# Optimization experiments

Measured on AMD Instinct MI355X. Metric: run time of the kernel, lower is better.

The kernel has to match this reference:

```python
import jax, jax.numpy as jnp
import numpy as np

# Dims: C cells, L gene tokens, E embed, H mlp hidden, M factors, K topk
C, L, E, H, M, K = 16, 8192, 512, 256, 128, 30
TAU = 1.0        # gumbel-softmax temperature
SOFTNESS = 0.01  # soft-mask sharpness
TEMP = 1.0       # logits temperature
EPS = 1e-20


def setup_inputs() -> dict:
    key = jax.random.key(0)
    ks = jax.random.split(key, 7)
    x = jax.random.normal(ks[0], (C, L, E), dtype=jnp.float32)
    key_padding_mask = jax.random.randint(ks[1], (C, L), 0, 2) > 0  # True = valid
    uniform_noise = jax.random.uniform(ks[2], (C, L - 1, M), dtype=jnp.float32)
    W1 = jax.random.normal(ks[3], (E, H), dtype=jnp.float32) * (1.0 / np.sqrt(E))
    b1 = jnp.zeros((H,), dtype=jnp.float32)
    W2 = jax.random.normal(ks[4], (H, M), dtype=jnp.float32) * (1.0 / np.sqrt(H))
    b2 = jnp.zeros((M,), dtype=jnp.float32)
    return {"x": x, "key_padding_mask": key_padding_mask,
            "uniform_noise": uniform_noise,
            "W1": W1, "b1": b1, "W2": W2, "b2": b2}


def reference(x, key_padding_mask, uniform_noise, W1, b1, W2, b2):
    # default gene_subset: drop token 0, keep the rest  -> S = L-1
    xs = x[:, 1:, :]                          # (C, S, E)
    kpm = key_padding_mask[:, 1:]             # (C, S)

    # 2-layer MLP router (dropout p=0 -> identity)
    h = jax.nn.relu(jnp.einsum('cse,eh->csh', xs, W1) + b1)   # (C, S, H)
    logits = (jnp.einsum('csh,hm->csm', h, W2) + b2) / TEMP    # (C, S, M)

    # GumbelTopK, training path: gumbel-softmax then smooth top-k mask
    gumbel = -jnp.log(-jnp.log(uniform_noise + EPS) + EPS)
    perturbed = (logits + gumbel) / TAU
    probs = jax.nn.softmax(perturbed, axis=-1)                 # (C, S, M)
    topk_vals, _ = jax.lax.top_k(probs, K)                     # (C, S, K)
    threshold = topk_vals[..., -1:]                            # (C, S, 1)
    smooth_mask = jax.nn.sigmoid((probs - threshold) / SOFTNESS)
    out = probs * smooth_mask

    # faithful to the source: mask = ~key_padding_mask; probs *= mask
    out = out * (~kpm)[..., None].astype(out.dtype)
    return out, kpm
```

## Files before the change

kernel.cpp:

```cpp
#include <hip/hip_runtime.h>
#include <hip/hip_bf16.h>

#define CC 16
#define LL 8192
#define SS 8191
#define EE 512
#define HH 256
#define MM 128
#define TOPK 30

typedef __attribute__((ext_vector_type(8))) short short8;
typedef __attribute__((ext_vector_type(4))) float f32x4;
typedef __attribute__((ext_vector_type(4))) unsigned int u32x4;

static __device__ __forceinline__ unsigned short f2bf(float f) {
    unsigned u = __builtin_bit_cast(unsigned, f);
    u += 0x7FFFu + ((u >> 16) & 1u);
    return (unsigned short)(u >> 16);
}

static __device__ __forceinline__ unsigned pk2(float lo, float hi) {
    __hip_bfloat162 t = __float22bfloat162_rn(float2{lo, hi});
    unsigned u;
    __builtin_memcpy(&u, &t, 4);
    return u;
}

static __device__ __forceinline__ short8 cvt8(const float4 a, const float4 b) {
    u32x4 uv;
    uv[0] = pk2(a.x, a.y);
    uv[1] = pk2(a.z, a.w);
    uv[2] = pk2(b.x, b.y);
    uv[3] = pk2(b.z, b.w);
    return __builtin_bit_cast(short8, uv);
}

template<int CTRL>
static __device__ __forceinline__ float dppf(float v) {
    return __builtin_bit_cast(float,
        __builtin_amdgcn_update_dpp(0, __builtin_bit_cast(int, v), CTRL, 0xF, 0xF, false));
}
template<int CTRL>
static __device__ __forceinline__ int dppi(int v) {
    return __builtin_amdgcn_update_dpp(0, v, CTRL, 0xF, 0xF, false);
}
static __device__ __forceinline__ float sum16f(float v) {
    v += dppf<0x121>(v); v += dppf<0x122>(v); v += dppf<0x124>(v); v += dppf<0x128>(v);
    return v;
}
static __device__ __forceinline__ float max16f(float v) {
    v = fmaxf(v, dppf<0x121>(v)); v = fmaxf(v, dppf<0x122>(v));
    v = fmaxf(v, dppf<0x124>(v)); v = fmaxf(v, dppf<0x128>(v));
    return v;
}
static __device__ __forceinline__ int sum16i(int v) {
    v += dppi<0x121>(v); v += dppi<0x122>(v); v += dppi<0x124>(v); v += dppi<0x128>(v);
    return v;
}

__global__ void prep_weights(const float* __restrict__ W1, const float* __restrict__ W2,
                             unsigned short* __restrict__ W1T, unsigned short* __restrict__ W2T)
{
    const int b = blockIdx.x, tid = threadIdx.x;
    if (b < 64) {
        const int e0 = b * 8, h = tid;
        short8 sv;
#pragma unroll
        for (int j = 0; j < 8; ++j)
            sv[j] = (short)f2bf(W1[(size_t)(e0 + j) * HH + h]);
        *(short8*)(void*)(W1T + (size_t)h * EE + e0) = sv;
    } else {
        const int h0 = (b - 64) * 16;
        if (tid < MM) {
            const int m = tid;
            short8 s0v, s1v;
#pragma unroll
            for (int j = 0; j < 8; ++j) {
                s0v[j] = (short)f2bf(W2[(size_t)(h0 + j) * MM + m]);
                s1v[j] = (short)f2bf(W2[(size_t)(h0 + 8 + j) * MM + m]);
            }
            *(short8*)(void*)(W2T + (size_t)m * HH + h0) = s0v;
            *(short8*)(void*)(W2T + (size_t)m * HH + h0 + 8) = s1v;
        }
    }
}

__global__ __launch_bounds__(256, 4)
void gene_router_kernel(const float* __restrict__ x,
                        const int*   __restrict__ mask,
                        const float* __restrict__ noise,
                        const unsigned short* __restrict__ W1T,
                        const float* __restrict__ b1,
                        const unsigned short* __restrict__ W2T,
                        const float* __restrict__ b2,
                        float* __restrict__ out,
                        float* __restrict__ outk)
{
    __shared__ __align__(16) unsigned char lds[32768];
    float* sLf = (float*)lds;

    const int tid = threadIdx.x;
    const int c   = blockIdx.y;
    const int s0  = blockIdx.x * 32;

    const int w    = tid >> 6;
    const int lane = tid & 63;
    const int lr   = lane & 15;
    const int kq   = lane >> 4;
    const int tx   = tid & 15;
    const int ty   = tid >> 4;

    if (tid < 32) {
        const int s = s0 + tid;
        if (s < SS)
            outk[(size_t)c * SS + s] = (mask[(size_t)c * LL + s + 1] != 0) ? 1.0f : 0.0f;
    }

    const float* xb = x + ((size_t)c * LL + s0 + 1) * EE;
    const int rowA = tid >> 5;
    const int cu   = tid & 31;
#pragma unroll
    for (int it = 0; it < 4; ++it) {
        const int row = it * 8 + rowA;
        const int rs  = min(s0 + row, SS - 1) - s0;
        const float* p = xb + (size_t)rs * EE + cu * 8;
        const float4 a = *(const float4*)p;
        const float4 b = *(const float4*)(p + 4);
        *(short8*)(void*)(lds + row * 512 + ((cu * 16) ^ ((row & 7) << 4))) = cvt8(a, b);
    }
    __syncthreads();

    float4 rB[4][2];
#pragma unroll
    for (int it = 0; it < 4; ++it) {
        const int row = it * 8 + rowA;
        const int rs  = min(s0 + row, SS - 1) - s0;
        const float* p = xb + (size_t)rs * EE + 256 + cu * 8;
        rB[it][0] = *(const float4*)p;
        rB[it][1] = *(const float4*)(p + 4);
    }

    const int cw = w * 64;
    float b1v[4];
#pragma unroll
    for (int n = 0; n < 4; ++n) b1v[n] = b1[cw + n * 16 + lr];

    f32x4 acc[2][4];
#pragma unroll
    for (int r = 0; r < 2; ++r)
#pragma unroll
        for (int n = 0; n < 4; ++n) acc[r][n] = (f32x4)0.0f;

#pragma unroll 4
    for (int ks2 = 0; ks2 < 8; ++ks2) {
        short8 af[2];
#pragma unroll
        for (int r = 0; r < 2; ++r) {
            const int row = r * 16 + lr;
            af[r] = *(const short8*)(const void*)(lds + row * 512
                        + ((ks2 * 64 + kq * 16) ^ ((row & 7) << 4)));
        }
        short8 bf_[4];
#pragma unroll
        for (int n = 0; n < 4; ++n)
            bf_[n] = *(const short8*)(const void*)(W1T + (size_t)(cw + n * 16 + lr) * EE + ks2 * 32 + kq * 8);
#pragma unroll
        for (int r = 0; r < 2; ++r)
#pragma unroll
            for (int n = 0; n < 4; ++n)
                acc[r][n] = __builtin_amdgcn_mfma_f32_16x16x32_bf16(af[r], bf_[n], acc[r][n], 0, 0, 0);
    }

#pragma unroll
    for (int it = 0; it < 4; ++it) {
        const int row = it * 8 + rowA;
        *(short8*)(void*)(lds + 16384 + row * 512 + ((cu * 16) ^ ((row & 7) << 4)))
            = cvt8(rB[it][0], rB[it][1]);
    }
    __syncthreads();

    float4 nz[2][2];
    int mk[2];
#pragma unroll
    for (int i = 0; i < 2; ++i) {
        const int s  = s0 + ty * 2 + i;
        const int sc = min(s, SS - 1);
        const float* np_ = noise + ((size_t)c * SS + sc) * MM + tx * 8;
        nz[i][0] = *(const float4*)np_;
        nz[i][1] = *(const float4*)(np_ + 4);
        mk[i] = mask[(size_t)c * LL + sc + 1];
    }
    const float4 b2a = *(const float4*)(b2 + tx * 8);
    const float4 b2b = *(const float4*)(b2 + tx * 8 + 4);

#pragma unroll 4
    for (int ks2 = 0; ks2 < 8; ++ks2) {
        short8 af[2];
#pragma unroll
        for (int r = 0; r < 2; ++r) {
            const int row = r * 16 + lr;
            af[r] = *(const short8*)(const void*)(lds + 16384 + row * 512
                        + ((ks2 * 64 + kq * 16) ^ ((row & 7) << 4)));
        }
        short8 bf_[4];
#pragma unroll
        for (int n = 0; n < 4; ++n)
            bf_[n] = *(const short8*)(const void*)(W1T + (size_t)(cw + n * 16 + lr) * EE + (8 + ks2) * 32 + kq * 8);
#pragma unroll
        for (int r = 0; r < 2; ++r)
#pragma unroll
            for (int n = 0; n < 4; ++n)
                acc[r][n] = __builtin_amdgcn_mfma_f32_16x16x32_bf16(af[r], bf_[n], acc[r][n], 0, 0, 0);
    }

#pragma unroll
    for (int n = 0; n < 4; ++n) {
        const int colh = cw + n * 16 + lr;
#pragma unroll
        for (int r = 0; r < 2; ++r)
#pragma unroll
            for (int q = 0; q < 4; ++q) {
                const int row = r * 16 + kq * 4 + q;
                const unsigned short hv = f2bf(fmaxf(acc[r][n][q] + b1v[n], 0.0f));
                *(unsigned short*)(lds + row * 512 + ((colh * 2) ^ ((row & 7) << 4))) = hv;
            }
    }
    __syncthreads();

    f32x4 acc2[2][2];
#pragma unroll
    for (int r = 0; r < 2; ++r)
#pragma unroll
        for (int n = 0; n < 2; ++n) acc2[r][n] = (f32x4)0.0f;

    const int cw2 = w * 32;
#pragma unroll 4
    for (int ks = 0; ks < 8; ++ks) {
        short8 ah[2];
#pragma unroll
        for (int r = 0; r < 2; ++r) {
            const int row = r * 16 + lr;
            ah[r] = *(const short8*)(const void*)(lds + row * 512
                        + ((ks * 64 + kq * 16) ^ ((row & 7) << 4)));
        }
        short8 bw[2];
#pragma unroll
        for (int n = 0; n < 2; ++n)
            bw[n] = *(const short8*)(const void*)(W2T + (size_t)(cw2 + n * 16 + lr) * HH + ks * 32 + kq * 8);
#pragma unroll
        for (int r = 0; r < 2; ++r)
#pragma unroll
            for (int n = 0; n < 2; ++n)
                acc2[r][n] = __builtin_amdgcn_mfma_f32_16x16x32_bf16(ah[r], bw[n], acc2[r][n], 0, 0, 0);
    }
    __syncthreads();

#pragma unroll
    for (int r = 0; r < 2; ++r)
#pragma unroll
        for (int n = 0; n < 2; ++n)
#pragma unroll
            for (int q = 0; q < 4; ++q) {
                const int row = r * 16 + kq * 4 + q;
                const int col = cw2 + n * 16 + lr;
                sLf[row * 132 + col] = acc2[r][n][q];
            }
    __syncthreads();

    float b2v[8] = {b2a.x, b2a.y, b2a.z, b2a.w, b2b.x, b2b.y, b2b.z, b2b.w};

    float pr[2][8];
    float pmaxv[2];
#pragma unroll
    for (int i = 0; i < 2; ++i) {
        const int row = ty * 2 + i;
        const float uu[8] = {nz[i][0].x, nz[i][0].y, nz[i][0].z, nz[i][0].w,
                             nz[i][1].x, nz[i][1].y, nz[i][1].z, nz[i][1].w};
        const float4 l0 = *(const float4*)&sLf[row * 132 + tx * 8];
        const float4 l1 = *(const float4*)&sLf[row * 132 + tx * 8 + 4];
        const float lg[8] = {l0.x, l0.y, l0.z, l0.w, l1.x, l1.y, l1.z, l1.w};
        float pm[8];
#pragma unroll
        for (int q = 0; q < 8; ++q) {
            const float g = -__logf(-__logf(uu[q] + 1e-20f) + 1e-20f);
            pm[q] = lg[q] + b2v[q] + g;
        }
        float mx = pm[0];
#pragma unroll
        for (int q = 1; q < 8; ++q) mx = fmaxf(mx, pm[q]);
        mx = max16f(mx);
        float se = 0.0f;
#pragma unroll
        for (int q = 0; q < 8; ++q) { pr[i][q] = __expf(pm[q] - mx); se += pr[i][q]; }
        se = sum16f(se);
        const float inv = 1.0f / se;
#pragma unroll
        for (int q = 0; q < 8; ++q) pr[i][q] *= inv;
        pmaxv[i] = inv;
    }

    float lo0 = 0.0f, lo1 = 0.0f;
    float hi0 = fminf(pmaxv[0], 1.0f / 30.0f);
    float hi1 = fminf(pmaxv[1], 1.0f / 30.0f);
    for (int it = 0; it < 16; ++it) {
        const float mid0 = 0.5f * (lo0 + hi0);
        const float mid1 = 0.5f * (lo1 + hi1);
        int cnt = 0;
#pragma unroll
        for (int q = 0; q < 8; ++q) {
            cnt += (pr[0][q] > mid0) ? 1 : 0;
            cnt += (pr[1][q] > mid1) ? 256 : 0;
        }
        cnt = sum16i(cnt);
        const bool ge0 = (cnt & 255) >= TOPK;
        const bool ge1 = (cnt >> 8)  >= TOPK;
        lo0 = ge0 ? mid0 : lo0;  hi0 = ge0 ? hi0 : mid0;
        lo1 = ge1 ? mid1 : lo1;  hi1 = ge1 ? hi1 : mid1;
    }
    const float thr_[2] = {hi0, hi1};

#pragma unroll
    for (int i = 0; i < 2; ++i) {
        const int s = s0 + ty * 2 + i;
        if (s < SS) {
            const float mz = (mk[i] != 0) ? 0.0f : 1.0f;
            float ov[8];
#pragma unroll
            for (int q = 0; q < 8; ++q) {
                const float sm = 1.0f / (1.0f + __expf((thr_[i] - pr[i][q]) * 100.0f));
                ov[q] = pr[i][q] * sm * mz;
            }
            float* op = out + ((size_t)c * SS + s) * MM + tx * 8;
            float4 o0, o1;
            o0.x=ov[0]; o0.y=ov[1]; o0.z=ov[2]; o0.w=ov[3];
            o1.x=ov[4]; o1.y=ov[5]; o1.z=ov[6]; o1.w=ov[7];
            *(float4*)(op + 0) = o0;
            *(float4*)(op + 4) = o1;
        }
    }
}

extern "C" void kernel_launch(void* const* d_in, const int* in_sizes, int n_in,
                              void* d_out, int out_size, void* d_ws, size_t ws_size,
                              hipStream_t stream) {
    const float* x     = (const float*)d_in[0];
    const int*   mask  = (const int*)d_in[1];
    const float* noise = (const float*)d_in[2];
    const float* W1    = (const float*)d_in[3];
    const float* b1    = (const float*)d_in[4];
    const float* W2    = (const float*)d_in[5];
    const float* b2    = (const float*)d_in[6];
    float* out  = (float*)d_out;
    float* outk = out + (size_t)CC * SS * MM;

    unsigned short* W1T = (unsigned short*)d_ws;
    unsigned short* W2T = W1T + (size_t)HH * EE;

    prep_weights<<<dim3(80), dim3(256), 0, stream>>>(W1, W2, W1T, W2T);

    dim3 grid(256, CC);
    gene_router_kernel<<<grid, dim3(256), 0, stream>>>(x, mask, noise, W1T, b1, W2T, b2, out, outk);
}
```

Baseline: 195.6 us.

## Retile router to 128-row blocks with double-buffered async global-to-LDS x staging

Each block now covers 128 sequence rows with 512 threads (8 waves laid out 2x4), so every W1/W2 fragment loaded from global is reused across four row tiles instead of two. The x tile is streamed in 64-column fp32 chunks straight into LDS with global_load_lds, double-buffered so the next chunk loads while MFMAs run on the current one, and the bf16 conversion moves to the LDS read side. The top-k bisection packs four rows' counts into one 32-bit DPP reduction. The cost is 64 KB of LDS per block, more accumulator registers and only 1024 blocks, which may reduce occupancy and latency hiding.

```diff
diff --git a/kernel.cpp b/kernel.cpp
--- a/kernel.cpp
+++ b/kernel.cpp
@@ -35,6 +35,13 @@
     return __builtin_bit_cast(short8, uv);
 }
 
+static __device__ __forceinline__ void gl2lds16(const float* g, unsigned char* l) {
+    __builtin_amdgcn_global_load_lds(
+        (const __attribute__((address_space(1))) void*)g,
+        (__attribute__((address_space(3))) void*)l,
+        16, 0, 0);
+}
+
 template<int CTRL>
 static __device__ __forceinline__ float dppf(float v) {
     return __builtin_bit_cast(float,
@@ -53,8 +60,9 @@
     v = fmaxf(v, dppf<0x124>(v)); v = fmaxf(v, dppf<0x128>(v));
     return v;
 }
-static __device__ __forceinline__ int sum16i(int v) {
-    v += dppi<0x121>(v); v += dppi<0x122>(v); v += dppi<0x124>(v); v += dppi<0x128>(v);
+static __device__ __forceinline__ unsigned sum16u(unsigned v) {
+    v += (unsigned)dppi<0x121>((int)v); v += (unsigned)dppi<0x122>((int)v);
+    v += (unsigned)dppi<0x124>((int)v); v += (unsigned)dppi<0x128>((int)v);
     return v;
 }
 
@@ -85,7 +93,7 @@
     }
 }
 
-__global__ __launch_bounds__(256, 4)
+__global__ __launch_bounds__(512, 4)
 void gene_router_kernel(const float* __restrict__ x,
                         const int*   __restrict__ mask,
                         const float* __restrict__ noise,
@@ -96,94 +104,102 @@
                         float* __restrict__ out,
                         float* __restrict__ outk)
 {
-    __shared__ __align__(16) unsigned char lds[32768];
-    float* sLf = (float*)lds;
+    __shared__ __align__(16) unsigned char lds[65536];
 
     const int tid = threadIdx.x;
     const int c   = blockIdx.y;
-    const int s0  = blockIdx.x * 32;
+    const int s0  = blockIdx.x * 128;
 
     const int w    = tid >> 6;
     const int lane = tid & 63;
     const int lr   = lane & 15;
     const int kq   = lane >> 4;
+    const int wr   = w >> 2;
+    const int wc   = w & 3;
     const int tx   = tid & 15;
     const int ty   = tid >> 4;
 
-    if (tid < 32) {
+    if (tid < 128) {
         const int s = s0 + tid;
         if (s < SS)
             outk[(size_t)c * SS + s] = (mask[(size_t)c * LL + s + 1] != 0) ? 1.0f : 0.0f;
     }
 
     const float* xb = x + ((size_t)c * LL + s0 + 1) * EE;
-    const int rowA = tid >> 5;
-    const int cu   = tid & 31;
-#pragma unroll
-    for (int it = 0; it < 4; ++it) {
-        const int row = it * 8 + rowA;
-        const int rs  = min(s0 + row, SS - 1) - s0;
-        const float* p = xb + (size_t)rs * EE + cu * 8;
-        const float4 a = *(const float4*)p;
-        const float4 b = *(const float4*)(p + 4);
-        *(short8*)(void*)(lds + row * 512 + ((cu * 16) ^ ((row & 7) << 4))) = cvt8(a, b);
-    }
+
+#define STAGE(ck, bufoff) do {                                              \
+    _Pragma("unroll")                                                       \
+    for (int it_ = 0; it_ < 4; ++it_) {                                     \
+        const int row_ = it_ * 32 + ty;                                     \
+        const int rs_  = min(s0 + row_, SS - 1) - s0;                       \
+        const float* g_ = xb + (size_t)rs_ * EE + (ck) * 64                 \
+                          + ((tx ^ (row_ & 7)) << 2);                       \
+        gl2lds16(g_, lds + (bufoff) + (it_ * 512 + tid) * 16);              \
+    } } while (0)
+
+    const int cw = wc * 64;
+    float b1v[4];
+#pragma unroll
+    for (int n = 0; n < 4; ++n) b1v[n] = b1[cw + n * 16 + lr];
+
+    f32x4 acc[4][4];
+#pragma unroll
+    for (int r = 0; r < 4; ++r)
+#pragma unroll
+        for (int n = 0; n < 4; ++n) acc[r][n] = (f32x4)0.0f;
+
+    STAGE(0, 0);
     __syncthreads();
 
-    float4 rB[4][2];
-#pragma unroll
-    for (int it = 0; it < 4; ++it) {
-        const int row = it * 8 + rowA;
-        const int rs  = min(s0 + row, SS - 1) - s0;
-        const float* p = xb + (size_t)rs * EE + 256 + cu * 8;
-        rB[it][0] = *(const float4*)p;
-        rB[it][1] = *(const float4*)(p + 4);
-    }
-
-    const int cw = w * 64;
-    float b1v[4];
-#pragma unroll
-    for (int n = 0; n < 4; ++n) b1v[n] = b1[cw + n * 16 + lr];
-
-    f32x4 acc[2][4];
-#pragma unroll
-    for (int r = 0; r < 2; ++r)
-#pragma unroll
-        for (int n = 0; n < 4; ++n) acc[r][n] = (f32x4)0.0f;
-
-#pragma unroll 4
-    for (int ks2 = 0; ks2 < 8; ++ks2) {
-        short8 af[2];
-#pragma unroll
-        for (int r = 0; r < 2; ++r) {
-            const int row = r * 16 + lr;
-            af[r] = *(const short8*)(const void*)(lds + row * 512
-                        + ((ks2 * 64 + kq * 16) ^ ((row & 7) << 4)));
-        }
-        short8 bf_[4];
-#pragma unroll
-        for (int n = 0; n < 4; ++n)
-            bf_[n] = *(const short8*)(const void*)(W1T + (size_t)(cw + n * 16 + lr) * EE + ks2 * 32 + kq * 8);
-#pragma unroll
-        for (int r = 0; r < 2; ++r)
+    for (int ck = 0; ck < 8; ++ck) {
+        const int cur = (ck & 1) << 15;
+        if (ck < 7) STAGE(ck + 1, ((ck + 1) & 1) << 15);
+#pragma unroll
+        for (int ks = 0; ks < 2; ++ks) {
+            short8 af[4];
+#pragma unroll
+            for (int r = 0; r < 4; ++r) {
+                const int row = wr * 64 + r * 16 + lr;
+                const int ug  = ks * 8 + kq * 2;
+                const float4 a0 = *(const float4*)(const void*)
+                    (lds + cur + row * 256 + (((ug + 0) ^ (row & 7)) << 4));
+                const float4 a1 = *(const float4*)(const void*)
+                    (lds + cur + row * 256 + (((ug + 1) ^ (row & 7)) << 4));
+                af[r] = cvt8(a0, a1);
+            }
+            short8 bf_[4];
 #pragma unroll
             for (int n = 0; n < 4; ++n)
-                acc[r][n] = __builtin_amdgcn_mfma_f32_16x16x32_bf16(af[r], bf_[n], acc[r][n], 0, 0, 0);
-    }
-
-#pragma unroll
-    for (int it = 0; it < 4; ++it) {
-        const int row = it * 8 + rowA;
-        *(short8*)(void*)(lds + 16384 + row * 512 + ((cu * 16) ^ ((row & 7) << 4)))
-            = cvt8(rB[it][0], rB[it][1]);
+                bf_[n] = *(const short8*)(const void*)
+                    (W1T + (size_t)(cw + n * 16 + lr) * EE + ck * 64 + ks * 32 + kq * 8);
+#pragma unroll
+            for (int r = 0; r < 4; ++r)
+#pragma unroll
+                for (int n = 0; n < 4; ++n)
+                    acc[r][n] = __builtin_amdgcn_mfma_f32_16x16x32_bf16(af[r], bf_[n], acc[r][n], 0, 0, 0);
+        }
+        __syncthreads();
+    }
+
+#pragma unroll
+    for (int n = 0; n < 4; ++n) {
+        const int colh = cw + n * 16 + lr;
+#pragma unroll
+        for (int r = 0; r < 4; ++r)
+#pragma unroll
+            for (int q = 0; q < 4; ++q) {
+                const int row = wr * 64 + r * 16 + kq * 4 + q;
+                *(unsigned short*)(lds + row * 512 + ((colh * 2) ^ ((row & 7) << 4))) =
+                    f2bf(fmaxf(acc[r][n][q] + b1v[n], 0.0f));
+            }
     }
     __syncthreads();
 
-    float4 nz[2][2];
-    int mk[2];
-#pragma unroll
-    for (int i = 0; i < 2; ++i) {
-        const int s  = s0 + ty * 2 + i;
+    float4 nz[4][2];
+    int mk[4];
+#pragma unroll
+    for (int i = 0; i < 4; ++i) {
+        const int s  = s0 + ty * 4 + i;
         const int sc = min(s, SS - 1);
         const float* np_ = noise + ((size_t)c * SS + sc) * MM + tx * 8;
         nz[i][0] = *(const float4*)np_;
@@ -193,62 +209,29 @@
     const float4 b2a = *(const float4*)(b2 + tx * 8);
     const float4 b2b = *(const float4*)(b2 + tx * 8 + 4);
 
-#pragma unroll 4
-    for (int ks2 = 0; ks2 < 8; ++ks2) {
-        short8 af[2];
-#pragma unroll
-        for (int r = 0; r < 2; ++r) {
-            const int row = r * 16 + lr;
-            af[r] = *(const short8*)(const void*)(lds + 16384 + row * 512
-                        + ((ks2 * 64 + kq * 16) ^ ((row & 7) << 4)));
-        }
-        short8 bf_[4];
-#pragma unroll
-        for (int n = 0; n < 4; ++n)
-            bf_[n] = *(const short8*)(const void*)(W1T + (size_t)(cw + n * 16 + lr) * EE + (8 + ks2) * 32 + kq * 8);
-#pragma unroll
-        for (int r = 0; r < 2; ++r)
-#pragma unroll
-            for (int n = 0; n < 4; ++n)
-                acc[r][n] = __builtin_amdgcn_mfma_f32_16x16x32_bf16(af[r], bf_[n], acc[r][n], 0, 0, 0);
-    }
-
-#pragma unroll
-    for (int n = 0; n < 4; ++n) {
-        const int colh = cw + n * 16 + lr;
-#pragma unroll
-        for (int r = 0; r < 2; ++r)
-#pragma unroll
-            for (int q = 0; q < 4; ++q) {
-                const int row = r * 16 + kq * 4 + q;
-                const unsigned short hv = f2bf(fmaxf(acc[r][n][q] + b1v[n], 0.0f));
-                *(unsigned short*)(lds + row * 512 + ((colh * 2) ^ ((row & 7) << 4))) = hv;
-            }
-    }
-    __syncthreads();
-
-    f32x4 acc2[2][2];
-#pragma unroll
-    for (int r = 0; r < 2; ++r)
+    f32x4 acc2[4][2];
+#pragma unroll
+    for (int r = 0; r < 4; ++r)
 #pragma unroll
         for (int n = 0; n < 2; ++n) acc2[r][n] = (f32x4)0.0f;
 
-    const int cw2 = w * 32;
+    const int cw2 = wc * 32;
 #pragma unroll 4
     for (int ks = 0; ks < 8; ++ks) {
-        short8 ah[2];
-#pragma unroll
-        for (int r = 0; r < 2; ++r) {
-            const int row = r * 16 + lr;
-            ah[r] = *(const short8*)(const void*)(lds + row * 512
-                        + ((ks * 64 + kq * 16) ^ ((row & 7) << 4)));
+        short8 ah[4];
+#pragma unroll
+        for (int r = 0; r < 4; ++r) {
+            const int row = wr * 64 + r * 16 + lr;
+            ah[r] = *(const short8*)(const void*)
+                (lds + row * 512 + ((ks * 64 + kq * 16) ^ ((row & 7) << 4)));
         }
         short8 bw[2];
 #pragma unroll
         for (int n = 0; n < 2; ++n)
-            bw[n] = *(const short8*)(const void*)(W2T + (size_t)(cw2 + n * 16 + lr) * HH + ks * 32 + kq * 8);
-#pragma unroll
-        for (int r = 0; r < 2; ++r)
+            bw[n] = *(const short8*)(const void*)
+                (W2T + (size_t)(cw2 + n * 16 + lr) * HH + ks * 32 + kq * 8);
+#pragma unroll
+        for (int r = 0; r < 4; ++r)
 #pragma unroll
             for (int n = 0; n < 2; ++n)
                 acc2[r][n] = __builtin_amdgcn_mfma_f32_16x16x32_bf16(ah[r], bw[n], acc2[r][n], 0, 0, 0);
@@ -256,29 +239,33 @@
     __syncthreads();
 
 #pragma unroll
-    for (int r = 0; r < 2; ++r)
+    for (int r = 0; r < 4; ++r)
 #pragma unroll
         for (int n = 0; n < 2; ++n)
 #pragma unroll
             for (int q = 0; q < 4; ++q) {
-                const int row = r * 16 + kq * 4 + q;
+                const int row = wr * 64 + r * 16 + kq * 4 + q;
                 const int col = cw2 + n * 16 + lr;
-                sLf[row * 132 + col] = acc2[r][n][q];
+                *(float*)(lds + row * 512
+                          + ((((col >> 2) << 4) ^ ((row & 7) << 4)) | ((col & 3) << 2)))
+                    = acc2[r][n][q];
             }
     __syncthreads();
 
     float b2v[8] = {b2a.x, b2a.y, b2a.z, b2a.w, b2b.x, b2b.y, b2b.z, b2b.w};
 
-    float pr[2][8];
-    float pmaxv[2];
-#pragma unroll
-    for (int i = 0; i < 2; ++i) {
-        const int row = ty * 2 + i;
+    float pr[4][8];
+    float pmaxv[4];
+#pragma unroll
+    for (int i = 0; i < 4; ++i) {
+        const int row = ty * 4 + i;
+        const float4 l0 = *(const float4*)(const void*)
+            (lds + row * 512 + ((tx * 32) ^ ((row & 7) << 4)));
+        const float4 l1 = *(const float4*)(const void*)
+            (lds + row * 512 + ((tx * 32 + 16) ^ ((row & 7) << 4)));
+        const float lg[8] = {l0.x, l0.y, l0.z, l0.w, l1.x, l1.y, l1.z, l1.w};
         const float uu[8] = {nz[i][0].x, nz[i][0].y, nz[i][0].z, nz[i][0].w,
                              nz[i][1].x, nz[i][1].y, nz[i][1].z, nz[i][1].w};
-        const float4 l0 = *(const float4*)&sLf[row * 132 + tx * 8];
-        const float4 l1 = *(const float4*)&sLf[row * 132 + tx * 8 + 4];
-        const float lg[8] = {l0.x, l0.y, l0.z, l0.w, l1.x, l1.y, l1.z, l1.w};
         float pm[8];
 #pragma unroll
         for (int q = 0; q < 8; ++q) {
@@ -299,35 +286,39 @@
         pmaxv[i] = inv;
     }
 
-    float lo0 = 0.0f, lo1 = 0.0f;
-    float hi0 = fminf(pmaxv[0], 1.0f / 30.0f);
-    float hi1 = fminf(pmaxv[1], 1.0f / 30.0f);
+    float lo[4], hi[4];
+#pragma unroll
+    for (int i = 0; i < 4; ++i) { lo[i] = 0.0f; hi[i] = fminf(pmaxv[i], 1.0f / 30.0f); }
     for (int it = 0; it < 16; ++it) {
-        const float mid0 = 0.5f * (lo0 + hi0);
-        const float mid1 = 0.5f * (lo1 + hi1);
-        int cnt = 0;
+        float mid[4];
+#pragma unroll
+        for (int i = 0; i < 4; ++i) mid[i] = 0.5f * (lo[i] + hi[i]);
+        unsigned cnt = 0;
 #pragma unroll
         for (int q = 0; q < 8; ++q) {
-            cnt += (pr[0][q] > mid0) ? 1 : 0;
-            cnt += (pr[1][q] > mid1) ? 256 : 0;
-        }
-        cnt = sum16i(cnt);
-        const bool ge0 = (cnt & 255) >= TOPK;
-        const bool ge1 = (cnt >> 8)  >= TOPK;
-        lo0 = ge0 ? mid0 : lo0;  hi0 = ge0 ? hi0 : mid0;
-        lo1 = ge1 ? mid1 : lo1;  hi1 = ge1 ? hi1 : mid1;
-    }
-    const float thr_[2] = {hi0, hi1};
-
-#pragma unroll
-    for (int i = 0; i < 2; ++i) {
-        const int s = s0 + ty * 2 + i;
+            cnt += (pr[0][q] > mid[0]) ? 1u : 0u;
+            cnt += (pr[1][q] > mid[1]) ? (1u << 8) : 0u;
+            cnt += (pr[2][q] > mid[2]) ? (1u << 16) : 0u;
+            cnt += (pr[3][q] > mid[3]) ? (1u << 24) : 0u;
+        }
+        cnt = sum16u(cnt);
+#pragma unroll
+        for (int i = 0; i < 4; ++i) {
+            const bool ge = ((cnt >> (8 * i)) & 255u) >= TOPK;
+            lo[i] = ge ? mid[i] : lo[i];
+            hi[i] = ge ? hi[i] : mid[i];
+        }
+    }
+
+#pragma unroll
+    for (int i = 0; i < 4; ++i) {
+        const int s = s0 + ty * 4 + i;
         if (s < SS) {
             const float mz = (mk[i] != 0) ? 0.0f : 1.0f;
             float ov[8];
 #pragma unroll
             for (int q = 0; q < 8; ++q) {
-                const float sm = 1.0f / (1.0f + __expf((thr_[i] - pr[i][q]) * 100.0f));
+                const float sm = 1.0f / (1.0f + __expf((hi[i] - pr[i][q]) * 100.0f));
                 ov[q] = pr[i][q] * sm * mz;
             }
             float* op = out + ((size_t)c * SS + s) * MM + tx * 8;
@@ -338,6 +329,7 @@
             *(float4*)(op + 4) = o1;
         }
     }
+#undef STAGE
 }
 
 extern "C" void kernel_launch(void* const* d_in, const int* in_sizes, int n_in,
@@ -358,6 +350,6 @@
 
     prep_weights<<<dim3(80), dim3(256), 0, stream>>>(W1, W2, W1T, W2T);
 
-    dim3 grid(256, CC);
-    gene_router_kernel<<<grid, dim3(256), 0, stream>>>(x, mask, noise, W1T, b1, W2T, b2, out, outk);
-}
+    dim3 grid(64, CC);
+    gene_router_kernel<<<grid, dim3(512), 0, stream>>>(x, mask, noise, W1T, b1, W2T, b2, out, outk);
+}
```

Result: faster. 181.0 us (-7.5%).
